# Kernel tuning notes

Measured on AMD Instinct MI355X. Metric: run time of the kernel, lower is better.

## Reference

```python
import jax, jax.numpy as jnp
import numpy as np

D = 256
H = 8
DH = D // H
N = 100000
B = 256
T = 131072
HID_FUSE = 256   # fuse MLP hidden = d_model
HID_HEAD = 256   # QuantileHeads hidden
NQ = 3           # quantiles (q10, q50, q90)


def setup_inputs() -> dict:
    key = jax.random.key(0)
    ks = jax.random.split(key, 32)
    p = lambda k, *s: (0.02 * jax.random.normal(k, s, dtype=jnp.float32))
    inp = {
        'node_embeddings': jax.random.normal(ks[0], (N, D), dtype=jnp.float32),
        'target_index': jax.random.randint(ks[1], (B,), 0, N),
        'port_index': jax.random.randint(ks[2], (T,), 0, N),
        'port_batch': jnp.sort(jax.random.randint(ks[3], (T,), 0, B)),
        'port_weight': jax.random.uniform(ks[4], (T,), dtype=jnp.float32),
        # PMA pooling params (learnable seed + MHA projections, no biases)
        'seed': p(ks[5], D),
        'Wq_p': p(ks[6], D, D), 'Wk_p': p(ks[7], D, D), 'Wv_p': p(ks[8], D, D), 'Wo_p': p(ks[9], D, D),
        # target->portfolio cross-attention params
        'Wq_c': p(ks[10], D, D), 'Wk_c': p(ks[11], D, D), 'Wv_c': p(ks[12], D, D), 'Wo_c': p(ks[13], D, D),
        # fuse LayerNorm(3d) + MLP
        'ln_g': jnp.ones((3 * D,), jnp.float32), 'ln_b': jnp.zeros((3 * D,), jnp.float32),
        'fuse_W1': p(ks[14], 3 * D, HID_FUSE), 'fuse_b1': jnp.zeros((HID_FUSE,), jnp.float32),
        'fuse_W2': p(ks[15], HID_FUSE, D), 'fuse_b2': jnp.zeros((D,), jnp.float32),
        # quantile heads MLP
        'head_W1': p(ks[16], D, HID_HEAD), 'head_b1': jnp.zeros((HID_HEAD,), jnp.float32),
        'head_W2': p(ks[17], HID_HEAD, NQ), 'head_b2': jnp.zeros((NQ,), jnp.float32),
    }
    return inp


def _segment_attend(logits, v, seg, num_segments):
    # logits [T,H], v [T,H,DH], seg [T] -> pooled [num_segments, H, DH]
    m = jax.ops.segment_max(logits, seg, num_segments=num_segments)  # [B,H]
    e = jnp.exp(logits - m[seg])                                      # [T,H]
    s = jax.ops.segment_sum(e, seg, num_segments=num_segments)        # [B,H]
    p = e / (s[seg] + 1e-9)
    return jax.ops.segment_sum(p[..., None] * v, seg, num_segments=num_segments)


def reference(node_embeddings, target_index, port_index, port_batch, port_weight,
              seed, Wq_p, Wk_p, Wv_p, Wo_p, Wq_c, Wk_c, Wv_c, Wo_c,
              ln_g, ln_b, fuse_W1, fuse_b1, fuse_W2, fuse_b2,
              head_W1, head_b1, head_W2, head_b2):
    b = target_index.shape[0]
    scale = float(DH) ** -0.5
    tgt = node_embeddings[target_index]          # [B,D]
    tok = node_embeddings[port_index]            # [T,D]
    logw = jnp.log(port_weight + 1e-8)           # DV01 weighting as logit bias

    # --- PMA: learnable seed query pools DV01-weighted portfolio tokens ---
    q_p = (seed @ Wq_p).reshape(H, DH)
    k_p = (tok @ Wk_p).reshape(-1, H, DH)
    v_p = (tok @ Wv_p).reshape(-1, H, DH)
    lg_p = jnp.einsum('thd,hd->th', k_p, q_p) * scale + logw[:, None]
    pooled = _segment_attend(lg_p, v_p, port_batch, b).reshape(b, D)
    contexts = pooled @ Wo_p                     # [B,D]; zeros for empty portfolios

    # --- target -> portfolio cross-attention (residual) ---
    q_c = (tgt @ Wq_c).reshape(b, H, DH)
    k_c = (tok @ Wk_c).reshape(-1, H, DH)
    v_c = (tok @ Wv_c).reshape(-1, H, DH)
    lg_c = jnp.einsum('thd,thd->th', k_c, q_c[port_batch]) * scale + logw[:, None]
    att = _segment_attend(lg_c, v_c, port_batch, b).reshape(b, D)
    fused = tgt + att @ Wo_c                     # [B,D]; == tgt for empty portfolios

    # --- fuse: concat -> LN -> MLP ---
    z = jnp.concatenate([tgt, contexts, fused], axis=-1)  # [B,3D]
    mu = jnp.mean(z, axis=-1, keepdims=True)
    var = jnp.var(z, axis=-1, keepdims=True)
    z = (z - mu) * jax.lax.rsqrt(var + 1e-5) * ln_g + ln_b
    z = jax.nn.relu(z @ fuse_W1 + fuse_b1) @ fuse_W2 + fuse_b2  # [B,D]

    # --- quantile heads ---
    out = jax.nn.relu(z @ head_W1 + head_b1) @ head_W2 + head_b2  # [B,NQ]
    return out
```

## Files before the change

kernel.cpp:

```cpp
#include <hip/hip_runtime.h>
#include <hip/hip_bf16.h>

typedef __attribute__((ext_vector_type(8))) short short8;
typedef __attribute__((ext_vector_type(4))) float floatx4;

#define SCALE 0.17677669529663687f

__device__ __forceinline__ unsigned short f2bf(float f) {
  unsigned int x = __float_as_uint(f);
  x += 0x7fffu + ((x >> 16) & 1u);
  return (unsigned short)(x >> 16);
}
__device__ __forceinline__ float bf2f(unsigned short u) {
  return __uint_as_float(((unsigned int)u) << 16);
}

__device__ __forceinline__ short8 load_cvt8(const float* p) {
  floatx4 a = *(const floatx4*)p;
  floatx4 b = *(const floatx4*)(p + 4);
  short8 r;
  r[0] = (short)f2bf(a[0]); r[1] = (short)f2bf(a[1]);
  r[2] = (short)f2bf(a[2]); r[3] = (short)f2bf(a[3]);
  r[4] = (short)f2bf(b[0]); r[5] = (short)f2bf(b[1]);
  r[6] = (short)f2bf(b[2]); r[7] = (short)f2bf(b[3]);
  return r;
}

__device__ __forceinline__ float block_sum(float v, float* red) {
  #pragma unroll
  for (int off = 32; off >= 1; off >>= 1) v += __shfl_xor(v, off, 64);
  __syncthreads();
  if ((threadIdx.x & 63) == 0) red[threadIdx.x >> 6] = v;
  __syncthreads();
  return red[0] + red[1] + red[2] + red[3];
}

__device__ __forceinline__ void matvec256(const float* __restrict__ W,
                                          const float* act, float* outv,
                                          float* red4, int tid) {
  const int c4 = tid & 63, kg = tid >> 6, c0 = c4 * 4;
  floatx4 acc = (floatx4){0.f, 0.f, 0.f, 0.f};
  const float* Wp = W + (size_t)(kg * 64) * 256 + c0;
  const float* ap = act + kg * 64;
  #pragma unroll 8
  for (int k = 0; k < 64; ++k) {
    floatx4 wv = *(const floatx4*)(Wp + (size_t)k * 256);
    float a = ap[k];
    acc[0] += a * wv[0]; acc[1] += a * wv[1];
    acc[2] += a * wv[2]; acc[3] += a * wv[3];
  }
  *(floatx4*)(red4 + kg * 256 + c0) = acc;
  __syncthreads();
  outv[tid] = red4[tid] + red4[256 + tid] + red4[512 + tid] + red4[768 + tid];
  __syncthreads();
}

__global__ __launch_bounds__(256) void setup_kernel(
    const float* __restrict__ node,
    const int* __restrict__ tgt_idx,
    const int* __restrict__ port_batch,
    const float* __restrict__ seed,
    const float* __restrict__ Wq_p,
    const float* __restrict__ Wk_p,
    const float* __restrict__ Wq_c,
    const float* __restrict__ Wk_c,
    unsigned short* __restrict__ u_p_t,
    unsigned short* __restrict__ u_c_all,
    int* __restrict__ seg, int T, int B)
{
  __shared__ float act_l[256];
  __shared__ float q_l[256];
  __shared__ __align__(16) float red4[1024];
  const int tid = threadIdx.x;
  const int b = blockIdx.x;

  if (tid == 0 || (tid == 64 && b == B - 1)) {
    int key = (tid == 0) ? b : B;
    int lo = 0, hi = T;
    while (lo < hi) { int mid = (lo + hi) >> 1; if (port_batch[mid] < key) lo = mid + 1; else hi = mid; }
    seg[key] = lo;
  }

  act_l[tid] = node[(size_t)tgt_idx[b] * 256 + tid];
  __syncthreads();
  matvec256(Wq_c, act_l, q_l, red4, tid);

  {
    float hs[8];
    #pragma unroll
    for (int h = 0; h < 8; ++h) hs[h] = 0.f;
    #pragma unroll
    for (int c = 0; c < 32; ++c) {
      floatx4 wa = *(const floatx4*)(Wk_c + (size_t)tid * 256 + c * 8);
      floatx4 wb = *(const floatx4*)(Wk_c + (size_t)tid * 256 + c * 8 + 4);
      const int h = c >> 2;
      #pragma unroll
      for (int j = 0; j < 4; ++j) hs[h] += wa[j] * q_l[c * 8 + j];
      #pragma unroll
      for (int j = 0; j < 4; ++j) hs[h] += wb[j] * q_l[c * 8 + 4 + j];
    }
    #pragma unroll
    for (int h = 0; h < 8; ++h)
      u_c_all[(size_t)b * 2048 + h * 256 + tid] = f2bf(hs[h]);
  }

  if (b == 0) {
    __syncthreads();
    act_l[tid] = seed[tid];
    __syncthreads();
    matvec256(Wq_p, act_l, q_l, red4, tid);
    float hs[8];
    #pragma unroll
    for (int h = 0; h < 8; ++h) hs[h] = 0.f;
    #pragma unroll
    for (int c = 0; c < 32; ++c) {
      floatx4 wa = *(const floatx4*)(Wk_p + (size_t)tid * 256 + c * 8);
      floatx4 wb = *(const floatx4*)(Wk_p + (size_t)tid * 256 + c * 8 + 4);
      const int h = c >> 2;
      #pragma unroll
      for (int j = 0; j < 4; ++j) hs[h] += wa[j] * q_l[c * 8 + j];
      #pragma unroll
      for (int j = 0; j < 4; ++j) hs[h] += wb[j] * q_l[c * 8 + 4 + j];
    }
    #pragma unroll
    for (int h = 0; h < 8; ++h) u_p_t[h * 256 + tid] = f2bf(hs[h]);
  }
}

__global__ __launch_bounds__(256, 3) void attn_kernel(
    const float* __restrict__ node,
    const int* __restrict__ port_index,
    const float* __restrict__ port_weight,
    const unsigned short* __restrict__ u_p_t,
    const unsigned short* __restrict__ u_c_all,
    const int* __restrict__ seg,
    float* __restrict__ slabs, int T, int S)
{
  __shared__ __align__(16) unsigned short tok_lds[64 * 264];
  __shared__ __align__(16) unsigned short E_t[16 * 72];
  __shared__ float l_lds[16];

  const int tid  = threadIdx.x;
  const int s    = blockIdx.x;
  const int b    = blockIdx.y;
  const int lane = tid & 63;
  const int w    = tid >> 6;
  const int q    = lane >> 4;
  const int n    = lane & 15;

  if (tid < 16) l_lds[tid] = 0.f;

  short8 ufrag[8];
  const unsigned short* ubase = (n < 8) ? (u_p_t + n * 256)
                                        : (u_c_all + (size_t)b * 2048 + (n - 8) * 256);
  #pragma unroll
  for (int s8 = 0; s8 < 8; ++s8)
    ufrag[s8] = *(const short8*)(ubase + q * 8 + s8 * 32);

  const int start  = seg[b];
  const int end    = seg[b + 1];
  const int ntiles = (end - start + 63) >> 6;

  floatx4 sacc[4];
  #pragma unroll
  for (int nt = 0; nt < 4; ++nt) sacc[nt] = (floatx4){0.f, 0.f, 0.f, 0.f};

  short8 cur[8], nxt[8];
  float pwc[4], pwn[4];

  __syncthreads();

  if (s < ntiles) {
    int t = start + s * 64 + w * 16 + n; int tc = t < T ? t : T - 1;
    const float* rp = node + (size_t)port_index[tc] * 256 + q * 8;
    #pragma unroll
    for (int k = 0; k < 8; ++k) cur[k] = load_cvt8(rp + k * 32);
    #pragma unroll
    for (int r = 0; r < 4; ++r) { int tr = start + s * 64 + w * 16 + q * 4 + r; pwc[r] = port_weight[tr < T ? tr : T - 1]; }
  }

  for (int it = s; it < ntiles; it += S) {
    const int tbase = start + it * 64;
    if (it + S < ntiles) {
      int t = start + (it + S) * 64 + w * 16 + n; int tc = t < T ? t : T - 1;
      const float* rp = node + (size_t)port_index[tc] * 256 + q * 8;
      #pragma unroll
      for (int k = 0; k < 8; ++k) nxt[k] = load_cvt8(rp + k * 32);
      #pragma unroll
      for (int r = 0; r < 4; ++r) { int tr = start + (it + S) * 64 + w * 16 + q * 4 + r; pwn[r] = port_weight[tr < T ? tr : T - 1]; }
    }
    floatx4 lacc = (floatx4){0.f, 0.f, 0.f, 0.f};
    #pragma unroll
    for (int k = 0; k < 8; ++k)
      lacc = __builtin_amdgcn_mfma_f32_16x16x32_bf16(cur[k], ufrag[k], lacc, 0, 0, 0);
    float lsum = 0.f;
    #pragma unroll
    for (int r = 0; r < 4; ++r) {
      const int tr = tbase + w * 16 + q * 4 + r;
      float e = 0.f;
      if (tr < end) {
        float lg = lacc[r] * SCALE + logf(pwc[r] + 1e-8f);
        e = __expf(lg);
      }
      unsigned short eb = f2bf(e);
      E_t[n * 72 + w * 16 + q * 4 + r] = eb;
      lsum += bf2f(eb);
    }
    lsum += __shfl_xor(lsum, 16, 64);
    lsum += __shfl_xor(lsum, 32, 64);
    if (lane < 16) atomicAdd(&l_lds[lane], lsum);
    #pragma unroll
    for (int k = 0; k < 8; ++k)
      *(short8*)(tok_lds + (w * 16 + n) * 264 + q * 8 + k * 32) = cur[k];
    __syncthreads();
    short8 ea0 = *(const short8*)(E_t + n * 72 + q * 8);
    short8 ea1 = *(const short8*)(E_t + n * 72 + 32 + q * 8);
    #pragma unroll
    for (int nt = 0; nt < 4; ++nt) {
      const int dcol = w * 64 + nt * 16 + n;
      short8 b0, b1;
      #pragma unroll
      for (int j = 0; j < 8; ++j) b0[j] = (short)tok_lds[(q * 8 + j) * 264 + dcol];
      #pragma unroll
      for (int j = 0; j < 8; ++j) b1[j] = (short)tok_lds[(32 + q * 8 + j) * 264 + dcol];
      sacc[nt] = __builtin_amdgcn_mfma_f32_16x16x32_bf16(ea0, b0, sacc[nt], 0, 0, 0);
      sacc[nt] = __builtin_amdgcn_mfma_f32_16x16x32_bf16(ea1, b1, sacc[nt], 0, 0, 0);
    }
    __syncthreads();
    #pragma unroll
    for (int k = 0; k < 8; ++k) cur[k] = nxt[k];
    #pragma unroll
    for (int r = 0; r < 4; ++r) pwc[r] = pwn[r];
  }

  float* sl = slabs + ((size_t)b * S + s) * 4224;
  #pragma unroll
  for (int nt = 0; nt < 4; ++nt)
    #pragma unroll
    for (int r = 0; r < 4; ++r)
      sl[(q * 4 + r) * 256 + w * 64 + nt * 16 + n] = sacc[nt][r];
  if (tid < 16) sl[4096 + tid] = l_lds[tid];
}

__global__ __launch_bounds__(256) void finalize_kernel(
    const float* __restrict__ node,
    const int* __restrict__ tgt_idx,
    const float* __restrict__ Wv_p,
    const float* __restrict__ Wo_p,
    const float* __restrict__ Wv_c,
    const float* __restrict__ Wo_c,
    const float* __restrict__ ln_g,
    const float* __restrict__ ln_b,
    const float* __restrict__ fuse_W1,
    const float* __restrict__ fuse_b1,
    const float* __restrict__ fuse_W2,
    const float* __restrict__ fuse_b2,
    const float* __restrict__ head_W1,
    const float* __restrict__ head_b1,
    const float* __restrict__ head_W2,
    const float* __restrict__ head_b2,
    const float* __restrict__ slabs,
    float* __restrict__ out, int S)
{
  __shared__ float s_lds[16 * 257];
  __shared__ float tgt_l[256];
  __shared__ float va[256], vb[256];
  __shared__ float z_l[768], zn_l[768];
  __shared__ __align__(16) float red4[1024];
  __shared__ float red_l[4];
  __shared__ float l_loc[16];

  const int tid = threadIdx.x;
  const int b   = blockIdx.x;
  const int c4 = tid & 63, kg = tid >> 6, c0 = c4 * 4;

  const float* sb = slabs + (size_t)b * S * 4224;
  for (int i = tid; i < 4096; i += 256) {
    float v = 0.f;
    for (int s = 0; s < S; ++s) v += sb[s * 4224 + i];
    s_lds[(i >> 8) * 257 + (i & 255)] = v;
  }
  if (tid < 16) {
    float v = 0.f;
    for (int s = 0; s < S; ++s) v += sb[s * 4224 + 4096 + tid];
    l_loc[tid] = v;
  }
  tgt_l[tid] = node[(size_t)tgt_idx[b] * 256 + tid];
  __syncthreads();
  #pragma unroll
  for (int r = 0; r < 16; ++r)
    s_lds[r * 257 + tid] *= 1.0f / (l_loc[r] + 1e-9f);
  __syncthreads();

  {
    const int hrow = c0 >> 5;
    floatx4 accP = (floatx4){0.f,0.f,0.f,0.f}, accA = accP;
    const float* wp = Wv_p + (size_t)(kg * 64) * 256 + c0;
    const float* wc = Wv_c + (size_t)(kg * 64) * 256 + c0;
    const float* ap = s_lds + hrow * 257 + kg * 64;
    const float* aa = s_lds + (8 + hrow) * 257 + kg * 64;
    #pragma unroll 8
    for (int k = 0; k < 64; ++k) {
      floatx4 w1 = *(const floatx4*)(wp + (size_t)k * 256);
      floatx4 w2 = *(const floatx4*)(wc + (size_t)k * 256);
      float a1 = ap[k], a2 = aa[k];
      accP[0] += a1*w1[0]; accP[1] += a1*w1[1]; accP[2] += a1*w1[2]; accP[3] += a1*w1[3];
      accA[0] += a2*w2[0]; accA[1] += a2*w2[1]; accA[2] += a2*w2[2]; accA[3] += a2*w2[3];
    }
    *(floatx4*)(red4 + kg * 256 + c0) = accP;
    __syncthreads();
    float po = red4[tid] + red4[256 + tid] + red4[512 + tid] + red4[768 + tid];
    __syncthreads();
    *(floatx4*)(red4 + kg * 256 + c0) = accA;
    __syncthreads();
    float ao = red4[tid] + red4[256 + tid] + red4[512 + tid] + red4[768 + tid];
    va[tid] = po; vb[tid] = ao;
    __syncthreads();
  }
  {
    floatx4 accP = (floatx4){0.f,0.f,0.f,0.f}, accA = accP;
    const float* wp = Wo_p + (size_t)(kg * 64) * 256 + c0;
    const float* wc = Wo_c + (size_t)(kg * 64) * 256 + c0;
    #pragma unroll 8
    for (int k = 0; k < 64; ++k) {
      floatx4 w1 = *(const floatx4*)(wp + (size_t)k * 256);
      floatx4 w2 = *(const floatx4*)(wc + (size_t)k * 256);
      float a1 = va[kg * 64 + k], a2 = vb[kg * 64 + k];
      accP[0] += a1*w1[0]; accP[1] += a1*w1[1]; accP[2] += a1*w1[2]; accP[3] += a1*w1[3];
      accA[0] += a2*w2[0]; accA[1] += a2*w2[1]; accA[2] += a2*w2[2]; accA[3] += a2*w2[3];
    }
    *(floatx4*)(red4 + kg * 256 + c0) = accP;
    __syncthreads();
    float cx = red4[tid] + red4[256 + tid] + red4[512 + tid] + red4[768 + tid];
    __syncthreads();
    *(floatx4*)(red4 + kg * 256 + c0) = accA;
    __syncthreads();
    float at2 = red4[tid] + red4[256 + tid] + red4[512 + tid] + red4[768 + tid];
    const float tg = tgt_l[tid];
    z_l[tid] = tg; z_l[256 + tid] = cx; z_l[512 + tid] = tg + at2;
    __syncthreads();
  }
  {
    const float z0 = z_l[tid], z1 = z_l[256 + tid], z2v = z_l[512 + tid];
    const float mu = block_sum(z0 + z1 + z2v, red_l) * (1.0f / 768.0f);
    const float d0 = z0 - mu, d1 = z1 - mu, d2 = z2v - mu;
    const float var = block_sum(d0 * d0 + d1 * d1 + d2 * d2, red_l) * (1.0f / 768.0f);
    const float rstd = 1.0f / sqrtf(var + 1e-5f);
    zn_l[tid]       = d0 * rstd * ln_g[tid]       + ln_b[tid];
    zn_l[256 + tid] = d1 * rstd * ln_g[256 + tid] + ln_b[256 + tid];
    zn_l[512 + tid] = d2 * rstd * ln_g[512 + tid] + ln_b[512 + tid];
    __syncthreads();
  }
  {
    floatx4 acc = (floatx4){0.f,0.f,0.f,0.f};
    const float* wp = fuse_W1 + (size_t)(kg * 192) * 256 + c0;
    const float* ap = zn_l + kg * 192;
    #pragma unroll 8
    for (int k = 0; k < 192; ++k) {
      floatx4 wv = *(const floatx4*)(wp + (size_t)k * 256);
      float a = ap[k];
      acc[0] += a*wv[0]; acc[1] += a*wv[1]; acc[2] += a*wv[2]; acc[3] += a*wv[3];
    }
    *(floatx4*)(red4 + kg * 256 + c0) = acc;
    __syncthreads();
    va[tid] = fmaxf(red4[tid] + red4[256 + tid] + red4[512 + tid] + red4[768 + tid] + fuse_b1[tid], 0.f);
    __syncthreads();
  }
  matvec256(fuse_W2, va, vb, red4, tid);
  {
    vb[tid] += fuse_b2[tid];
    __syncthreads();
  }
  matvec256(head_W1, vb, va, red4, tid);
  {
    va[tid] = fmaxf(va[tid] + head_b1[tid], 0.f);
    __syncthreads();
  }
  #pragma unroll
  for (int q2 = 0; q2 < 3; ++q2) {
    float p = va[tid] * head_W2[tid * 3 + q2];
    float tot = block_sum(p, red_l);
    if (tid == 0) out[b * 3 + q2] = tot + head_b2[q2];
  }
}

extern "C" void kernel_launch(void* const* d_in, const int* in_sizes, int n_in,
                              void* d_out, int out_size, void* d_ws, size_t ws_size,
                              hipStream_t stream) {
  const float* node        = (const float*)d_in[0];
  const int*   tgt_idx     = (const int*)d_in[1];
  const int*   port_index  = (const int*)d_in[2];
  const int*   port_batch  = (const int*)d_in[3];
  const float* port_weight = (const float*)d_in[4];
  const float* seed        = (const float*)d_in[5];
  const float* Wq_p = (const float*)d_in[6];
  const float* Wk_p = (const float*)d_in[7];
  const float* Wv_p = (const float*)d_in[8];
  const float* Wo_p = (const float*)d_in[9];
  const float* Wq_c = (const float*)d_in[10];
  const float* Wk_c = (const float*)d_in[11];
  const float* Wv_c = (const float*)d_in[12];
  const float* Wo_c = (const float*)d_in[13];
  const float* ln_g = (const float*)d_in[14];
  const float* ln_b = (const float*)d_in[15];
  const float* fuse_W1 = (const float*)d_in[16];
  const float* fuse_b1 = (const float*)d_in[17];
  const float* fuse_W2 = (const float*)d_in[18];
  const float* fuse_b2 = (const float*)d_in[19];
  const float* head_W1 = (const float*)d_in[20];
  const float* head_b1 = (const float*)d_in[21];
  const float* head_W2 = (const float*)d_in[22];
  const float* head_b2 = (const float*)d_in[23];

  const int B = in_sizes[1];
  const int T = in_sizes[2];

  unsigned short* u_p_t   = (unsigned short*)d_ws;
  int*            seg     = (int*)((char*)d_ws + 4096);
  unsigned short* u_c_all = (unsigned short*)((char*)d_ws + 8192);
  size_t slab_off = 8192 + (size_t)B * 4096;
  float* slabs = (float*)((char*)d_ws + slab_off);
  size_t per_split = (size_t)B * 4224 * 4;
  int S = 1;
  if (ws_size >= slab_off + 4 * per_split) S = 4;
  else if (ws_size >= slab_off + 2 * per_split) S = 2;

  setup_kernel<<<B, 256, 0, stream>>>(node, tgt_idx, port_batch, seed,
      Wq_p, Wk_p, Wq_c, Wk_c, u_p_t, u_c_all, seg, T, B);
  attn_kernel<<<dim3(S, B), 256, 0, stream>>>(node, port_index, port_weight,
      u_p_t, u_c_all, seg, slabs, T, S);
  finalize_kernel<<<B, 256, 0, stream>>>(node, tgt_idx,
      Wv_p, Wo_p, Wv_c, Wo_c, ln_g, ln_b,
      fuse_W1, fuse_b1, fuse_W2, fuse_b2, head_W1, head_b1, head_W2, head_b2,
      slabs, (float*)d_out, S);
}
```

Before: 320.7 us.

## Split finalize into batched multi-kernel GEMM chain and raise attention occupancy

The single per-batch finalize kernel, which streams every weight matrix once per batch row, is replaced by a chain of six small kernels. Each processes four batch rows per block across 16 column tiles, so weights are reused across rows and many more blocks run at once. The attention kernel's launch bound goes from 3 to 4 waves per SIMD, and the split count S now scales up to 8 with available workspace. The cost is extra launches, intermediate buffers round-tripping through global memory, and scalar strided weight loads, plus possible register spills in the attention kernel.

```diff
diff --git a/kernel.cpp b/kernel.cpp
--- a/kernel.cpp
+++ b/kernel.cpp
@@ -24,15 +24,6 @@
   r[4] = (short)f2bf(b[0]); r[5] = (short)f2bf(b[1]);
   r[6] = (short)f2bf(b[2]); r[7] = (short)f2bf(b[3]);
   return r;
-}
-
-__device__ __forceinline__ float block_sum(float v, float* red) {
-  #pragma unroll
-  for (int off = 32; off >= 1; off >>= 1) v += __shfl_xor(v, off, 64);
-  __syncthreads();
-  if ((threadIdx.x & 63) == 0) red[threadIdx.x >> 6] = v;
-  __syncthreads();
-  return red[0] + red[1] + red[2] + red[3];
 }
 
 __device__ __forceinline__ void matvec256(const float* __restrict__ W,
@@ -127,7 +118,7 @@
   }
 }
 
-__global__ __launch_bounds__(256, 3) void attn_kernel(
+__global__ __launch_bounds__(256, 4) void attn_kernel(
     const float* __restrict__ node,
     const int* __restrict__ port_index,
     const float* __restrict__ port_weight,
@@ -242,145 +233,154 @@
   if (tid < 16) sl[4096 + tid] = l_lds[tid];
 }
 
-__global__ __launch_bounds__(256) void finalize_kernel(
-    const float* __restrict__ node,
-    const int* __restrict__ tgt_idx,
-    const float* __restrict__ Wv_p,
-    const float* __restrict__ Wo_p,
-    const float* __restrict__ Wv_c,
-    const float* __restrict__ Wo_c,
-    const float* __restrict__ ln_g,
-    const float* __restrict__ ln_b,
-    const float* __restrict__ fuse_W1,
-    const float* __restrict__ fuse_b1,
-    const float* __restrict__ fuse_W2,
-    const float* __restrict__ fuse_b2,
-    const float* __restrict__ head_W1,
-    const float* __restrict__ head_b1,
-    const float* __restrict__ head_W2,
-    const float* __restrict__ head_b2,
-    const float* __restrict__ slabs,
-    float* __restrict__ out, int S)
-{
-  __shared__ float s_lds[16 * 257];
-  __shared__ float tgt_l[256];
-  __shared__ float va[256], vb[256];
-  __shared__ float z_l[768], zn_l[768];
-  __shared__ __align__(16) float red4[1024];
-  __shared__ float red_l[4];
-  __shared__ float l_loc[16];
-
+__global__ __launch_bounds__(256) void k_slab_gemm(
+    const float* __restrict__ slabs, int S,
+    const float* __restrict__ Wv_p, const float* __restrict__ Wv_c,
+    float* __restrict__ X)
+{
+  __shared__ float act_l[4 * 256];
+  __shared__ float lsum[4];
   const int tid = threadIdx.x;
-  const int b   = blockIdx.x;
-  const int c4 = tid & 63, kg = tid >> 6, c0 = c4 * 4;
-
-  const float* sb = slabs + (size_t)b * S * 4224;
-  for (int i = tid; i < 4096; i += 256) {
+  const int bt = blockIdx.x, nt = blockIdx.y, z = blockIdx.z;
+  const int head = nt >> 1;
+  const int row = z * 8 + head;
+  if (tid < 4) {
+    const float* sl = slabs + (size_t)(bt * 4 + tid) * S * 4224;
+    float l = 0.f;
+    for (int s = 0; s < S; ++s) l += sl[s * 4224 + 4096 + row];
+    lsum[tid] = 1.0f / (l + 1e-9f);
+  }
+  __syncthreads();
+  for (int i = tid; i < 4 * 256; i += 256) {
+    int m = i >> 8, k = i & 255;
+    const float* sl = slabs + (size_t)(bt * 4 + m) * S * 4224;
+    float sum = 0.f;
+    for (int s = 0; s < S; ++s) sum += sl[s * 4224 + row * 256 + k];
+    act_l[i] = sum * lsum[m];
+  }
+  __syncthreads();
+  const int m = tid >> 6, lane = tid & 63, ks = lane >> 4, n = lane & 15;
+  const int n0 = nt * 16;
+  const float* W = z ? Wv_c : Wv_p;
+  float acc = 0.f;
+  const float* Wp = W + (size_t)(ks * 64) * 256 + n0 + n;
+  const float* ap = &act_l[m * 256 + ks * 64];
+  #pragma unroll 8
+  for (int k = 0; k < 64; ++k) acc += ap[k] * Wp[(size_t)k * 256];
+  acc += __shfl_xor(acc, 16, 64);
+  acc += __shfl_xor(acc, 32, 64);
+  if (ks == 0)
+    X[(size_t)(bt * 4 + m) * 512 + z * 256 + n0 + n] = acc;
+}
+
+__global__ __launch_bounds__(256) void k_plain_gemm(
+    const float* __restrict__ act, int act_ld,
+    const float* __restrict__ W0, const float* __restrict__ W1,
+    const float* __restrict__ bias0, const float* __restrict__ bias1,
+    float* __restrict__ outp, int out_ld,
+    int K, int relu)
+{
+  __shared__ float act_l[4 * 768];
+  const int tid = threadIdx.x;
+  const int bt = blockIdx.x, nt = blockIdx.y, z = blockIdx.z;
+  const float* W = z ? W1 : W0;
+  const float* bias = z ? bias1 : bias0;
+  for (int i = tid; i < 4 * K; i += 256) {
+    int m = i / K, k = i - m * K;
+    act_l[m * K + k] = act[(size_t)(bt * 4 + m) * act_ld + z * K + k];
+  }
+  __syncthreads();
+  const int m = tid >> 6, lane = tid & 63, ks = lane >> 4, n = lane & 15;
+  const int n0 = nt * 16;
+  const int Kq = K >> 2;
+  float acc = 0.f;
+  const float* Wp = W + (size_t)(ks * Kq) * 256 + n0 + n;
+  const float* ap = &act_l[m * K + ks * Kq];
+  #pragma unroll 8
+  for (int k = 0; k < Kq; ++k) acc += ap[k] * Wp[(size_t)k * 256];
+  acc += __shfl_xor(acc, 16, 64);
+  acc += __shfl_xor(acc, 32, 64);
+  if (ks == 0) {
+    float v = acc + (bias ? bias[n0 + n] : 0.f);
+    if (relu) v = fmaxf(v, 0.f);
+    outp[(size_t)(bt * 4 + m) * out_ld + z * 256 + n0 + n] = v;
+  }
+}
+
+__global__ __launch_bounds__(256) void k_ln_gemm(
+    const float* __restrict__ node, const int* __restrict__ tgt_idx,
+    const float* __restrict__ zbuf,
+    const float* __restrict__ ln_g, const float* __restrict__ ln_b,
+    const float* __restrict__ fuse_W1, const float* __restrict__ fuse_b1,
+    float* __restrict__ h1)
+{
+  __shared__ float act_l[4 * 768];
+  const int tid = threadIdx.x;
+  const int bt = blockIdx.x, nt = blockIdx.y;
+  for (int i = tid; i < 4 * 256; i += 256) {
+    int m = i >> 8, k = i & 255;
+    int b = bt * 4 + m;
+    float tg = node[(size_t)tgt_idx[b] * 256 + k];
+    float C  = zbuf[(size_t)b * 512 + k];
+    float Fp = zbuf[(size_t)b * 512 + 256 + k];
+    act_l[m * 768 + k]       = tg;
+    act_l[m * 768 + 256 + k] = C;
+    act_l[m * 768 + 512 + k] = tg + Fp;
+  }
+  __syncthreads();
+  const int m = tid >> 6, lane = tid & 63;
+  {
+    float s = 0.f;
+    for (int k = lane; k < 768; k += 64) s += act_l[m * 768 + k];
+    #pragma unroll
+    for (int o = 32; o >= 1; o >>= 1) s += __shfl_xor(s, o, 64);
+    const float mu = s * (1.0f / 768.0f);
     float v = 0.f;
-    for (int s = 0; s < S; ++s) v += sb[s * 4224 + i];
-    s_lds[(i >> 8) * 257 + (i & 255)] = v;
-  }
-  if (tid < 16) {
-    float v = 0.f;
-    for (int s = 0; s < S; ++s) v += sb[s * 4224 + 4096 + tid];
-    l_loc[tid] = v;
-  }
-  tgt_l[tid] = node[(size_t)tgt_idx[b] * 256 + tid];
-  __syncthreads();
+    for (int k = lane; k < 768; k += 64) { float d = act_l[m * 768 + k] - mu; v += d * d; }
+    #pragma unroll
+    for (int o = 32; o >= 1; o >>= 1) v += __shfl_xor(v, o, 64);
+    const float rstd = 1.0f / sqrtf(v * (1.0f / 768.0f) + 1e-5f);
+    for (int k = lane; k < 768; k += 64)
+      act_l[m * 768 + k] = (act_l[m * 768 + k] - mu) * rstd * ln_g[k] + ln_b[k];
+  }
+  __syncthreads();
+  const int ks = lane >> 4, n = lane & 15;
+  const int n0 = nt * 16;
+  float acc = 0.f;
+  const float* Wp = fuse_W1 + (size_t)(ks * 192) * 256 + n0 + n;
+  const float* ap = &act_l[m * 768 + ks * 192];
+  #pragma unroll 8
+  for (int k = 0; k < 192; ++k) acc += ap[k] * Wp[(size_t)k * 256];
+  acc += __shfl_xor(acc, 16, 64);
+  acc += __shfl_xor(acc, 32, 64);
+  if (ks == 0)
+    h1[(size_t)(bt * 4 + m) * 256 + n0 + n] = fmaxf(acc + fuse_b1[n0 + n], 0.f);
+}
+
+__global__ __launch_bounds__(256) void k_outhead(
+    const float* __restrict__ hh, const float* __restrict__ head_W2,
+    const float* __restrict__ head_b2, float* __restrict__ out)
+{
+  const int tid = threadIdx.x;
+  const int m = tid >> 6, lane = tid & 63;
+  const int b = blockIdx.x * 4 + m;
+  float a0 = 0.f, a1 = 0.f, a2 = 0.f;
+  for (int k = lane; k < 256; k += 64) {
+    float h = hh[(size_t)b * 256 + k];
+    a0 += h * head_W2[k * 3 + 0];
+    a1 += h * head_W2[k * 3 + 1];
+    a2 += h * head_W2[k * 3 + 2];
+  }
   #pragma unroll
-  for (int r = 0; r < 16; ++r)
-    s_lds[r * 257 + tid] *= 1.0f / (l_loc[r] + 1e-9f);
-  __syncthreads();
-
-  {
-    const int hrow = c0 >> 5;
-    floatx4 accP = (floatx4){0.f,0.f,0.f,0.f}, accA = accP;
-    const float* wp = Wv_p + (size_t)(kg * 64) * 256 + c0;
-    const float* wc = Wv_c + (size_t)(kg * 64) * 256 + c0;
-    const float* ap = s_lds + hrow * 257 + kg * 64;
-    const float* aa = s_lds + (8 + hrow) * 257 + kg * 64;
-    #pragma unroll 8
-    for (int k = 0; k < 64; ++k) {
-      floatx4 w1 = *(const floatx4*)(wp + (size_t)k * 256);
-      floatx4 w2 = *(const floatx4*)(wc + (size_t)k * 256);
-      float a1 = ap[k], a2 = aa[k];
-      accP[0] += a1*w1[0]; accP[1] += a1*w1[1]; accP[2] += a1*w1[2]; accP[3] += a1*w1[3];
-      accA[0] += a2*w2[0]; accA[1] += a2*w2[1]; accA[2] += a2*w2[2]; accA[3] += a2*w2[3];
-    }
-    *(floatx4*)(red4 + kg * 256 + c0) = accP;
-    __syncthreads();
-    float po = red4[tid] + red4[256 + tid] + red4[512 + tid] + red4[768 + tid];
-    __syncthreads();
-    *(floatx4*)(red4 + kg * 256 + c0) = accA;
-    __syncthreads();
-    float ao = red4[tid] + red4[256 + tid] + red4[512 + tid] + red4[768 + tid];
-    va[tid] = po; vb[tid] = ao;
-    __syncthreads();
-  }
-  {
-    floatx4 accP = (floatx4){0.f,0.f,0.f,0.f}, accA = accP;
-    const float* wp = Wo_p + (size_t)(kg * 64) * 256 + c0;
-    const float* wc = Wo_c + (size_t)(kg * 64) * 256 + c0;
-    #pragma unroll 8
-    for (int k = 0; k < 64; ++k) {
-      floatx4 w1 = *(const floatx4*)(wp + (size_t)k * 256);
-      floatx4 w2 = *(const floatx4*)(wc + (size_t)k * 256);
-      float a1 = va[kg * 64 + k], a2 = vb[kg * 64 + k];
-      accP[0] += a1*w1[0]; accP[1] += a1*w1[1]; accP[2] += a1*w1[2]; accP[3] += a1*w1[3];
-      accA[0] += a2*w2[0]; accA[1] += a2*w2[1]; accA[2] += a2*w2[2]; accA[3] += a2*w2[3];
-    }
-    *(floatx4*)(red4 + kg * 256 + c0) = accP;
-    __syncthreads();
-    float cx = red4[tid] + red4[256 + tid] + red4[512 + tid] + red4[768 + tid];
-    __syncthreads();
-    *(floatx4*)(red4 + kg * 256 + c0) = accA;
-    __syncthreads();
-    float at2 = red4[tid] + red4[256 + tid] + red4[512 + tid] + red4[768 + tid];
-    const float tg = tgt_l[tid];
-    z_l[tid] = tg; z_l[256 + tid] = cx; z_l[512 + tid] = tg + at2;
-    __syncthreads();
-  }
-  {
-    const float z0 = z_l[tid], z1 = z_l[256 + tid], z2v = z_l[512 + tid];
-    const float mu = block_sum(z0 + z1 + z2v, red_l) * (1.0f / 768.0f);
-    const float d0 = z0 - mu, d1 = z1 - mu, d2 = z2v - mu;
-    const float var = block_sum(d0 * d0 + d1 * d1 + d2 * d2, red_l) * (1.0f / 768.0f);
-    const float rstd = 1.0f / sqrtf(var + 1e-5f);
-    zn_l[tid]       = d0 * rstd * ln_g[tid]       + ln_b[tid];
-    zn_l[256 + tid] = d1 * rstd * ln_g[256 + tid] + ln_b[256 + tid];
-    zn_l[512 + tid] = d2 * rstd * ln_g[512 + tid] + ln_b[512 + tid];
-    __syncthreads();
-  }
-  {
-    floatx4 acc = (floatx4){0.f,0.f,0.f,0.f};
-    const float* wp = fuse_W1 + (size_t)(kg * 192) * 256 + c0;
-    const float* ap = zn_l + kg * 192;
-    #pragma unroll 8
-    for (int k = 0; k < 192; ++k) {
-      floatx4 wv = *(const floatx4*)(wp + (size_t)k * 256);
-      float a = ap[k];
-      acc[0] += a*wv[0]; acc[1] += a*wv[1]; acc[2] += a*wv[2]; acc[3] += a*wv[3];
-    }
-    *(floatx4*)(red4 + kg * 256 + c0) = acc;
-    __syncthreads();
-    va[tid] = fmaxf(red4[tid] + red4[256 + tid] + red4[512 + tid] + red4[768 + tid] + fuse_b1[tid], 0.f);
-    __syncthreads();
-  }
-  matvec256(fuse_W2, va, vb, red4, tid);
-  {
-    vb[tid] += fuse_b2[tid];
-    __syncthreads();
-  }
-  matvec256(head_W1, vb, va, red4, tid);
-  {
-    va[tid] = fmaxf(va[tid] + head_b1[tid], 0.f);
-    __syncthreads();
-  }
-  #pragma unroll
-  for (int q2 = 0; q2 < 3; ++q2) {
-    float p = va[tid] * head_W2[tid * 3 + q2];
-    float tot = block_sum(p, red_l);
-    if (tid == 0) out[b * 3 + q2] = tot + head_b2[q2];
+  for (int o = 32; o >= 1; o >>= 1) {
+    a0 += __shfl_xor(a0, o, 64);
+    a1 += __shfl_xor(a1, o, 64);
+    a2 += __shfl_xor(a2, o, 64);
+  }
+  if (lane == 0) {
+    out[b * 3 + 0] = a0 + head_b2[0];
+    out[b * 3 + 1] = a1 + head_b2[1];
+    out[b * 3 + 2] = a2 + head_b2[2];
   }
 }
 
@@ -415,22 +415,39 @@
   const int B = in_sizes[1];
   const int T = in_sizes[2];
 
-  unsigned short* u_p_t   = (unsigned short*)d_ws;
-  int*            seg     = (int*)((char*)d_ws + 4096);
-  unsigned short* u_c_all = (unsigned short*)((char*)d_ws + 8192);
+  char* ws = (char*)d_ws;
+  unsigned short* u_p_t   = (unsigned short*)ws;
+  int*            seg     = (int*)(ws + 4096);
+  unsigned short* u_c_all = (unsigned short*)(ws + 8192);
+  float* X    = (float*)(ws + 8192);
+  float* zbuf = (float*)(ws + 8192 + (size_t)B * 2048);
   size_t slab_off = 8192 + (size_t)B * 4096;
-  float* slabs = (float*)((char*)d_ws + slab_off);
-  size_t per_split = (size_t)B * 4224 * 4;
+  float* slabs = (float*)(ws + slab_off);
+  float* h1 = slabs;
+  float* z2 = h1 + (size_t)B * 256;
+  float* hh = z2 + (size_t)B * 256;
+
+  size_t per_slice = (size_t)B * 4224 * 4;
   int S = 1;
-  if (ws_size >= slab_off + 4 * per_split) S = 4;
-  else if (ws_size >= slab_off + 2 * per_split) S = 2;
+  if (ws_size > slab_off) {
+    size_t fit = (ws_size - slab_off) / per_slice;
+    S = (int)(fit < 1 ? 1 : (fit > 8 ? 8 : fit));
+  }
+
+  const int BT = B / 4;
 
   setup_kernel<<<B, 256, 0, stream>>>(node, tgt_idx, port_batch, seed,
       Wq_p, Wk_p, Wq_c, Wk_c, u_p_t, u_c_all, seg, T, B);
   attn_kernel<<<dim3(S, B), 256, 0, stream>>>(node, port_index, port_weight,
       u_p_t, u_c_all, seg, slabs, T, S);
-  finalize_kernel<<<B, 256, 0, stream>>>(node, tgt_idx,
-      Wv_p, Wo_p, Wv_c, Wo_c, ln_g, ln_b,
-      fuse_W1, fuse_b1, fuse_W2, fuse_b2, head_W1, head_b1, head_W2, head_b2,
-      slabs, (float*)d_out, S);
-}
+  k_slab_gemm<<<dim3(BT, 16, 2), 256, 0, stream>>>(slabs, S, Wv_p, Wv_c, X);
+  k_plain_gemm<<<dim3(BT, 16, 2), 256, 0, stream>>>(X, 512, Wo_p, Wo_c,
+      nullptr, nullptr, zbuf, 512, 256, 0);
+  k_ln_gemm<<<dim3(BT, 16), 256, 0, stream>>>(node, tgt_idx, zbuf,
+      ln_g, ln_b, fuse_W1, fuse_b1, h1);
+  k_plain_gemm<<<dim3(BT, 16, 1), 256, 0, stream>>>(h1, 256, fuse_W2, nullptr,
+      fuse_b2, nullptr, z2, 256, 256, 0);
+  k_plain_gemm<<<dim3(BT, 16, 1), 256, 0, stream>>>(z2, 256, head_W1, nullptr,
+      head_b1, nullptr, hh, 256, 256, 1);
+  k_outhead<<<BT, 256, 0, stream>>>(hh, head_W2, head_b2, (float*)d_out);
+}
```

After: 359.8 us. +12.2%, slower.
